# Optimization experiments

Measured on AMD Instinct MI355X. Metric: run time of the kernel, lower is better.

## Reference

```python
import jax, jax.numpy as jnp
import numpy as np

H = 4  # hidden_size
L = 2  # num_layers


def _lstm_cell(x, h, c, Wih, Whh, bih, bhh):
    # PyTorch gate order: input, forget, cell(g), output
    gates = x @ Wih.T + h @ Whh.T + (bih + bhh)  # [B, 4H]
    i, f, g, o = jnp.split(gates, 4, axis=-1)
    i = jax.nn.sigmoid(i)
    f = jax.nn.sigmoid(f)
    g = jnp.tanh(g)
    o = jax.nn.sigmoid(o)
    c_new = f * c + i * g
    h_new = o * jnp.tanh(c_new)
    return h_new, c_new


def setup_inputs() -> dict:
    key = jax.random.key(0)
    ks = jax.random.split(key, 24)
    B, S, D, T = 32768, 256, 8, 12
    s = 1.0 / np.sqrt(H)  # PyTorch LSTM init scale

    def u(k, shape):
        return jax.random.uniform(k, shape, jnp.float32, -s, s)

    inp = {
        "src": jax.random.normal(ks[0], (B, S, D), jnp.float32),
        "trg": jax.random.normal(ks[1], (B, T, 1), jnp.float32),
        # encoder LSTM (input_dim=8 -> H, then H -> H)
        "enc_Wih0": u(ks[2], (4 * H, D)), "enc_Whh0": u(ks[3], (4 * H, H)),
        "enc_bih0": u(ks[4], (4 * H,)), "enc_bhh0": u(ks[5], (4 * H,)),
        "enc_Wih1": u(ks[6], (4 * H, H)), "enc_Whh1": u(ks[7], (4 * H, H)),
        "enc_bih1": u(ks[8], (4 * H,)), "enc_bhh1": u(ks[9], (4 * H,)),
        # decoder LSTM (input_dim=1 -> H, then H -> H)
        "dec_Wih0": u(ks[10], (4 * H, 1)), "dec_Whh0": u(ks[11], (4 * H, H)),
        "dec_bih0": u(ks[12], (4 * H,)), "dec_bhh0": u(ks[13], (4 * H,)),
        "dec_Wih1": u(ks[14], (4 * H, H)), "dec_Whh1": u(ks[15], (4 * H, H)),
        "dec_bih1": u(ks[16], (4 * H,)), "dec_bhh1": u(ks[17], (4 * H,)),
        # fc: hidden -> 1
        "fc_W": u(ks[18], (1, H)), "fc_b": u(ks[19], (1,)),
    }
    return inp


def reference(src, trg,
              enc_Wih0, enc_Whh0, enc_bih0, enc_bhh0,
              enc_Wih1, enc_Whh1, enc_bih1, enc_bhh1,
              dec_Wih0, dec_Whh0, dec_bih0, dec_bhh0,
              dec_Wih1, dec_Whh1, dec_bih1, dec_bhh1,
              fc_W, fc_b):
    B, T = src.shape[0], trg.shape[1]
    enc_layers = [(enc_Wih0, enc_Whh0, enc_bih0, enc_bhh0),
                  (enc_Wih1, enc_Whh1, enc_bih1, enc_bhh1)]
    dec_layers = [(dec_Wih0, dec_Whh0, dec_bih0, dec_bhh0),
                  (dec_Wih1, dec_Whh1, dec_bih1, dec_bhh1)]

    def multi_step(layers, h, c, x):
        new_h, new_c, inp = [], [], x
        for l, p in enumerate(layers):
            hl, cl = _lstm_cell(inp, h[l], c[l], *p)
            new_h.append(hl); new_c.append(cl); inp = hl
        return jnp.stack(new_h), jnp.stack(new_c), inp

    # ---- encoder: scan over src time steps ----
    h0 = jnp.zeros((L, B, H), src.dtype)
    c0 = jnp.zeros((L, B, H), src.dtype)

    def enc_step(carry, x_t):
        h, c = carry
        h, c, _ = multi_step(enc_layers, h, c, x_t)
        return (h, c), None

    (h, c), _ = jax.lax.scan(enc_step, (h0, c0), jnp.swapaxes(src, 0, 1))

    x0 = trg[:, 0, :]  # [B, 1]

    def dec_step(carry, _):
        h, c, x = carry
        h, c, top = multi_step(dec_layers, h, c, x)
        pred = top @ fc_W.T + fc_b  # [B, 1]
        return (h, c, pred), pred

    _, preds = jax.lax.scan(dec_step, (h, c, x0), None, length=T - 1)  # [T-1, B, 1]
    outputs = jnp.concatenate([x0[None], preds], axis=0)  # [T, B, 1]
    return jnp.swapaxes(outputs, 0, 1)  # [B, T, 1]
```

## Files before the change

kernel.cpp:

```cpp
#include <hip/hip_runtime.h>

namespace {

constexpr int Sn = 256;
constexpr int Tn = 12;

__device__ __forceinline__ float rcp_(float x) { return __builtin_amdgcn_rcpf(x); }
__device__ __forceinline__ float sigm_(float x) { return rcp_(1.0f + __expf(-x)); }
__device__ __forceinline__ float tanh_(float x) { return 1.0f - 2.0f * rcp_(__expf(2.0f * x) + 1.0f); }

template <int CTRL>
__device__ __forceinline__ float qperm(float v) {
  return __int_as_float(
      __builtin_amdgcn_mov_dpp(__float_as_int(v), CTRL, 0xF, 0xF, true));
}
constexpr int DPP_XOR1 = 0xB1;
constexpr int DPP_XOR2 = 0x4E;
constexpr int DPP_XOR3 = 0x1B;
constexpr int DPP_BC0 = 0x00;

__device__ __forceinline__ float unit_update(const float* g, float& c) {
  float iv = sigm_(g[0]);
  float fv = sigm_(g[1]);
  float gv = tanh_(g[2]);
  float ov = sigm_(g[3]);
  c = fmaf(fv, c, iv * gv);
  return ov * tanh_(c);
}

__device__ __forceinline__ void quad_gather(float h, float* hg) {
  hg[0] = h;
  hg[1] = qperm<DPP_XOR1>(h);
  hg[2] = qperm<DPP_XOR2>(h);
  hg[3] = qperm<DPP_XOR3>(h);
}

__global__ __launch_bounds__(64) void seq2seq_kernel(
    const float* __restrict__ src, const float* __restrict__ trg,
    const float* __restrict__ eWih0, const float* __restrict__ eWhh0,
    const float* __restrict__ ebih0, const float* __restrict__ ebhh0,
    const float* __restrict__ eWih1, const float* __restrict__ eWhh1,
    const float* __restrict__ ebih1, const float* __restrict__ ebhh1,
    const float* __restrict__ dWih0, const float* __restrict__ dWhh0,
    const float* __restrict__ dbih0, const float* __restrict__ dbhh0,
    const float* __restrict__ dWih1, const float* __restrict__ dWhh1,
    const float* __restrict__ dbih1, const float* __restrict__ dbhh1,
    const float* __restrict__ fcW, const float* __restrict__ fcb,
    float* __restrict__ out) {
  const int gid = blockIdx.x * 64 + threadIdx.x;
  const int e = gid >> 2;
  const int u = gid & 3;

  float w0x[4][8], w0h[4][4], b0r[4];
  float w1i[4][4], w1h[4][4], b1r[4];
#pragma unroll
  for (int gi = 0; gi < 4; ++gi) {
    const int r = gi * 4 + u;
#pragma unroll
    for (int j = 0; j < 8; ++j) w0x[gi][j] = eWih0[r * 8 + j];
#pragma unroll
    for (int k = 0; k < 4; ++k) {
      w0h[gi][k] = eWhh0[r * 4 + (u ^ k)];
      w1i[gi][k] = eWih1[r * 4 + (u ^ k)];
      w1h[gi][k] = eWhh1[r * 4 + (u ^ k)];
    }
    b0r[gi] = ebih0[r] + ebhh0[r];
    b1r[gi] = ebih1[r] + ebhh1[r];
  }

  const float4* sp = (const float4*)(src + (size_t)e * (Sn * 8));

  float h0g[4] = {0, 0, 0, 0};
  float h1g[4] = {0, 0, 0, 0};
  float c0 = 0.0f, c1 = 0.0f;

  for (int t = 0; t < Sn; ++t) {
    float4 xa = sp[2 * t];
    float4 xb = sp[2 * t + 1];
    float x[8] = {xa.x, xa.y, xa.z, xa.w, xb.x, xb.y, xb.z, xb.w};
    float g[4];
#pragma unroll
    for (int gi = 0; gi < 4; ++gi) {
      float acc = b0r[gi];
#pragma unroll
      for (int j = 0; j < 8; ++j) acc = fmaf(x[j], w0x[gi][j], acc);
#pragma unroll
      for (int k = 0; k < 4; ++k) acc = fmaf(h0g[k], w0h[gi][k], acc);
      g[gi] = acc;
    }
    float h0 = unit_update(g, c0);
    quad_gather(h0, h0g);
#pragma unroll
    for (int gi = 0; gi < 4; ++gi) {
      float acc = b1r[gi];
#pragma unroll
      for (int k = 0; k < 4; ++k) acc = fmaf(h0g[k], w1i[gi][k], acc);
#pragma unroll
      for (int k = 0; k < 4; ++k) acc = fmaf(h1g[k], w1h[gi][k], acc);
      g[gi] = acc;
    }
    float h1 = unit_update(g, c1);
    quad_gather(h1, h1g);
  }

  float dw0i[4], dw0h[4][4], db0[4];
  float dw1i[4][4], dw1h[4][4], db1[4];
  float fcw[4];
#pragma unroll
  for (int gi = 0; gi < 4; ++gi) {
    const int r = gi * 4 + u;
    dw0i[gi] = dWih0[r];
#pragma unroll
    for (int k = 0; k < 4; ++k) {
      dw0h[gi][k] = dWhh0[r * 4 + (u ^ k)];
      dw1i[gi][k] = dWih1[r * 4 + (u ^ k)];
      dw1h[gi][k] = dWhh1[r * 4 + (u ^ k)];
    }
    db0[gi] = dbih0[r] + dbhh0[r];
    db1[gi] = dbih1[r] + dbhh1[r];
  }
#pragma unroll
  for (int k = 0; k < 4; ++k) fcw[k] = fcW[u ^ k];
  const float fcbv = fcb[0];

  float xv = trg[(size_t)e * Tn];
  if (u == 0) out[(size_t)e * Tn] = xv;

  for (int t = 1; t < Tn; ++t) {
    float g[4];
#pragma unroll
    for (int gi = 0; gi < 4; ++gi) {
      float acc = fmaf(xv, dw0i[gi], db0[gi]);
#pragma unroll
      for (int k = 0; k < 4; ++k) acc = fmaf(h0g[k], dw0h[gi][k], acc);
      g[gi] = acc;
    }
    float h0 = unit_update(g, c0);
    quad_gather(h0, h0g);
#pragma unroll
    for (int gi = 0; gi < 4; ++gi) {
      float acc = db1[gi];
#pragma unroll
      for (int k = 0; k < 4; ++k) acc = fmaf(h0g[k], dw1i[gi][k], acc);
#pragma unroll
      for (int k = 0; k < 4; ++k) acc = fmaf(h1g[k], dw1h[gi][k], acc);
      g[gi] = acc;
    }
    float h1 = unit_update(g, c1);
    quad_gather(h1, h1g);
    float pred = fcbv;
#pragma unroll
    for (int k = 0; k < 4; ++k) pred = fmaf(h1g[k], fcw[k], pred);
    pred = qperm<DPP_BC0>(pred);
    if (u == 0) out[(size_t)e * Tn + t] = pred;
    xv = pred;
  }
}

}

extern "C" void kernel_launch(void* const* d_in, const int* in_sizes, int n_in,
                              void* d_out, int out_size, void* d_ws, size_t ws_size,
                              hipStream_t stream) {
  const float* src = (const float*)d_in[0];
  const float* trg = (const float*)d_in[1];
  const float* eWih0 = (const float*)d_in[2];
  const float* eWhh0 = (const float*)d_in[3];
  const float* ebih0 = (const float*)d_in[4];
  const float* ebhh0 = (const float*)d_in[5];
  const float* eWih1 = (const float*)d_in[6];
  const float* eWhh1 = (const float*)d_in[7];
  const float* ebih1 = (const float*)d_in[8];
  const float* ebhh1 = (const float*)d_in[9];
  const float* dWih0 = (const float*)d_in[10];
  const float* dWhh0 = (const float*)d_in[11];
  const float* dbih0 = (const float*)d_in[12];
  const float* dbhh0 = (const float*)d_in[13];
  const float* dWih1 = (const float*)d_in[14];
  const float* dWhh1 = (const float*)d_in[15];
  const float* dbih1 = (const float*)d_in[16];
  const float* dbhh1 = (const float*)d_in[17];
  const float* fcW = (const float*)d_in[18];
  const float* fcb = (const float*)d_in[19];
  float* out = (float*)d_out;

  const int B = 32768;
  const int lanes = B * 4;
  const int block = 64;
  const int grid = lanes / block;
  seq2seq_kernel<<<grid, block, 0, stream>>>(
      src, trg, eWih0, eWhh0, ebih0, ebhh0, eWih1, eWhh1, ebih1, ebhh1,
      dWih0, dWhh0, dbih0, dbhh0, dWih1, dWhh1, dbih1, dbhh1, fcW, fcb, out);
}
```

Baseline: 544.1 us.

## Use packed FP32 FMA for LSTM gate math and prefetch next src step

Gate weights are regrouped into pairs (input/forget and cell/output) so the gate dot products run as packed two-wide FMAs (v_pk_fma_f32) instead of scalar FMAs, roughly halving the FMA instruction count per step. The encoder loop also loads the next time step's src vectors one iteration early to hide global-load latency behind compute. The costs are broadcast moves to build the packed operands, and more live registers from the prefetch and the paired weight layout.

```diff
diff --git a/kernel.cpp b/kernel.cpp
--- a/kernel.cpp
+++ b/kernel.cpp
@@ -4,6 +4,12 @@
 
 constexpr int Sn = 256;
 constexpr int Tn = 12;
+
+typedef float v2f __attribute__((ext_vector_type(2)));
+
+__device__ __forceinline__ v2f pkfma(v2f a, v2f b, v2f c) {
+  return __builtin_elementwise_fma(a, b, c);
+}
 
 __device__ __forceinline__ float rcp_(float x) { return __builtin_amdgcn_rcpf(x); }
 __device__ __forceinline__ float sigm_(float x) { return rcp_(1.0f + __expf(-x)); }
@@ -19,11 +25,11 @@
 constexpr int DPP_XOR3 = 0x1B;
 constexpr int DPP_BC0 = 0x00;
 
-__device__ __forceinline__ float unit_update(const float* g, float& c) {
-  float iv = sigm_(g[0]);
-  float fv = sigm_(g[1]);
-  float gv = tanh_(g[2]);
-  float ov = sigm_(g[3]);
+__device__ __forceinline__ float unit_update(v2f g01, v2f g23, float& c) {
+  float iv = sigm_(g01.x);
+  float fv = sigm_(g01.y);
+  float gv = tanh_(g23.x);
+  float ov = sigm_(g23.y);
   c = fmaf(fv, c, iv * gv);
   return ov * tanh_(c);
 }
@@ -51,22 +57,29 @@
   const int e = gid >> 2;
   const int u = gid & 3;
 
-  float w0x[4][8], w0h[4][4], b0r[4];
-  float w1i[4][4], w1h[4][4], b1r[4];
-#pragma unroll
-  for (int gi = 0; gi < 4; ++gi) {
-    const int r = gi * 4 + u;
-#pragma unroll
-    for (int j = 0; j < 8; ++j) w0x[gi][j] = eWih0[r * 8 + j];
-#pragma unroll
-    for (int k = 0; k < 4; ++k) {
-      w0h[gi][k] = eWhh0[r * 4 + (u ^ k)];
-      w1i[gi][k] = eWih1[r * 4 + (u ^ k)];
-      w1h[gi][k] = eWhh1[r * 4 + (u ^ k)];
-    }
-    b0r[gi] = ebih0[r] + ebhh0[r];
-    b1r[gi] = ebih1[r] + ebhh1[r];
-  }
+  const int ri = u, rf = 4 + u, rg = 8 + u, ro = 12 + u;
+
+  v2f w0x01[8], w0x23[8], w0h01[4], w0h23[4];
+  v2f w1i01[4], w1i23[4], w1h01[4], w1h23[4];
+#pragma unroll
+  for (int j = 0; j < 8; ++j) {
+    w0x01[j] = v2f{eWih0[ri * 8 + j], eWih0[rf * 8 + j]};
+    w0x23[j] = v2f{eWih0[rg * 8 + j], eWih0[ro * 8 + j]};
+  }
+#pragma unroll
+  for (int k = 0; k < 4; ++k) {
+    const int kc = u ^ k;
+    w0h01[k] = v2f{eWhh0[ri * 4 + kc], eWhh0[rf * 4 + kc]};
+    w0h23[k] = v2f{eWhh0[rg * 4 + kc], eWhh0[ro * 4 + kc]};
+    w1i01[k] = v2f{eWih1[ri * 4 + kc], eWih1[rf * 4 + kc]};
+    w1i23[k] = v2f{eWih1[rg * 4 + kc], eWih1[ro * 4 + kc]};
+    w1h01[k] = v2f{eWhh1[ri * 4 + kc], eWhh1[rf * 4 + kc]};
+    w1h23[k] = v2f{eWhh1[rg * 4 + kc], eWhh1[ro * 4 + kc]};
+  }
+  const v2f b0_01 = v2f{ebih0[ri] + ebhh0[ri], ebih0[rf] + ebhh0[rf]};
+  const v2f b0_23 = v2f{ebih0[rg] + ebhh0[rg], ebih0[ro] + ebhh0[ro]};
+  const v2f b1_01 = v2f{ebih1[ri] + ebhh1[ri], ebih1[rf] + ebhh1[rf]};
+  const v2f b1_23 = v2f{ebih1[rg] + ebhh1[rg], ebih1[ro] + ebhh1[ro]};
 
   const float4* sp = (const float4*)(src + (size_t)e * (Sn * 8));
 
@@ -74,51 +87,65 @@
   float h1g[4] = {0, 0, 0, 0};
   float c0 = 0.0f, c1 = 0.0f;
 
+  float4 xa = sp[0], xb = sp[1];
   for (int t = 0; t < Sn; ++t) {
-    float4 xa = sp[2 * t];
-    float4 xb = sp[2 * t + 1];
+    const int tn = (t < Sn - 1) ? t + 1 : t;
+    float4 na = sp[2 * tn];
+    float4 nb = sp[2 * tn + 1];
+
     float x[8] = {xa.x, xa.y, xa.z, xa.w, xb.x, xb.y, xb.z, xb.w};
-    float g[4];
-#pragma unroll
-    for (int gi = 0; gi < 4; ++gi) {
-      float acc = b0r[gi];
-#pragma unroll
-      for (int j = 0; j < 8; ++j) acc = fmaf(x[j], w0x[gi][j], acc);
-#pragma unroll
-      for (int k = 0; k < 4; ++k) acc = fmaf(h0g[k], w0h[gi][k], acc);
-      g[gi] = acc;
-    }
-    float h0 = unit_update(g, c0);
+    v2f a01 = b0_01, a23 = b0_23;
+#pragma unroll
+    for (int j = 0; j < 8; ++j) {
+      v2f xx = v2f{x[j], x[j]};
+      a01 = pkfma(xx, w0x01[j], a01);
+      a23 = pkfma(xx, w0x23[j], a23);
+    }
+#pragma unroll
+    for (int k = 0; k < 4; ++k) {
+      v2f hh = v2f{h0g[k], h0g[k]};
+      a01 = pkfma(hh, w0h01[k], a01);
+      a23 = pkfma(hh, w0h23[k], a23);
+    }
+    float h0 = unit_update(a01, a23, c0);
     quad_gather(h0, h0g);
-#pragma unroll
-    for (int gi = 0; gi < 4; ++gi) {
-      float acc = b1r[gi];
-#pragma unroll
-      for (int k = 0; k < 4; ++k) acc = fmaf(h0g[k], w1i[gi][k], acc);
-#pragma unroll
-      for (int k = 0; k < 4; ++k) acc = fmaf(h1g[k], w1h[gi][k], acc);
-      g[gi] = acc;
-    }
-    float h1 = unit_update(g, c1);
+
+    a01 = b1_01;
+    a23 = b1_23;
+#pragma unroll
+    for (int k = 0; k < 4; ++k) {
+      v2f hh0 = v2f{h0g[k], h0g[k]};
+      v2f hh1 = v2f{h1g[k], h1g[k]};
+      a01 = pkfma(hh0, w1i01[k], a01);
+      a23 = pkfma(hh0, w1i23[k], a23);
+      a01 = pkfma(hh1, w1h01[k], a01);
+      a23 = pkfma(hh1, w1h23[k], a23);
+    }
+    float h1 = unit_update(a01, a23, c1);
     quad_gather(h1, h1g);
-  }
-
-  float dw0i[4], dw0h[4][4], db0[4];
-  float dw1i[4][4], dw1h[4][4], db1[4];
+
+    xa = na;
+    xb = nb;
+  }
+
+  v2f dw0i01 = v2f{dWih0[ri], dWih0[rf]};
+  v2f dw0i23 = v2f{dWih0[rg], dWih0[ro]};
+  v2f dw0h01[4], dw0h23[4], dw1i01[4], dw1i23[4], dw1h01[4], dw1h23[4];
+#pragma unroll
+  for (int k = 0; k < 4; ++k) {
+    const int kc = u ^ k;
+    dw0h01[k] = v2f{dWhh0[ri * 4 + kc], dWhh0[rf * 4 + kc]};
+    dw0h23[k] = v2f{dWhh0[rg * 4 + kc], dWhh0[ro * 4 + kc]};
+    dw1i01[k] = v2f{dWih1[ri * 4 + kc], dWih1[rf * 4 + kc]};
+    dw1i23[k] = v2f{dWih1[rg * 4 + kc], dWih1[ro * 4 + kc]};
+    dw1h01[k] = v2f{dWhh1[ri * 4 + kc], dWhh1[rf * 4 + kc]};
+    dw1h23[k] = v2f{dWhh1[rg * 4 + kc], dWhh1[ro * 4 + kc]};
+  }
+  const v2f db0_01 = v2f{dbih0[ri] + dbhh0[ri], dbih0[rf] + dbhh0[rf]};
+  const v2f db0_23 = v2f{dbih0[rg] + dbhh0[rg], dbih0[ro] + dbhh0[ro]};
+  const v2f db1_01 = v2f{dbih1[ri] + dbhh1[ri], dbih1[rf] + dbhh1[rf]};
+  const v2f db1_23 = v2f{dbih1[rg] + dbhh1[rg], dbih1[ro] + dbhh1[ro]};
   float fcw[4];
-#pragma unroll
-  for (int gi = 0; gi < 4; ++gi) {
-    const int r = gi * 4 + u;
-    dw0i[gi] = dWih0[r];
-#pragma unroll
-    for (int k = 0; k < 4; ++k) {
-      dw0h[gi][k] = dWhh0[r * 4 + (u ^ k)];
-      dw1i[gi][k] = dWih1[r * 4 + (u ^ k)];
-      dw1h[gi][k] = dWhh1[r * 4 + (u ^ k)];
-    }
-    db0[gi] = dbih0[r] + dbhh0[r];
-    db1[gi] = dbih1[r] + dbhh1[r];
-  }
 #pragma unroll
   for (int k = 0; k < 4; ++k) fcw[k] = fcW[u ^ k];
   const float fcbv = fcb[0];
@@ -127,27 +154,32 @@
   if (u == 0) out[(size_t)e * Tn] = xv;
 
   for (int t = 1; t < Tn; ++t) {
-    float g[4];
-#pragma unroll
-    for (int gi = 0; gi < 4; ++gi) {
-      float acc = fmaf(xv, dw0i[gi], db0[gi]);
-#pragma unroll
-      for (int k = 0; k < 4; ++k) acc = fmaf(h0g[k], dw0h[gi][k], acc);
-      g[gi] = acc;
-    }
-    float h0 = unit_update(g, c0);
+    v2f xx = v2f{xv, xv};
+    v2f a01 = pkfma(xx, dw0i01, db0_01);
+    v2f a23 = pkfma(xx, dw0i23, db0_23);
+#pragma unroll
+    for (int k = 0; k < 4; ++k) {
+      v2f hh = v2f{h0g[k], h0g[k]};
+      a01 = pkfma(hh, dw0h01[k], a01);
+      a23 = pkfma(hh, dw0h23[k], a23);
+    }
+    float h0 = unit_update(a01, a23, c0);
     quad_gather(h0, h0g);
-#pragma unroll
-    for (int gi = 0; gi < 4; ++gi) {
-      float acc = db1[gi];
-#pragma unroll
-      for (int k = 0; k < 4; ++k) acc = fmaf(h0g[k], dw1i[gi][k], acc);
-#pragma unroll
-      for (int k = 0; k < 4; ++k) acc = fmaf(h1g[k], dw1h[gi][k], acc);
-      g[gi] = acc;
-    }
-    float h1 = unit_update(g, c1);
+
+    a01 = db1_01;
+    a23 = db1_23;
+#pragma unroll
+    for (int k = 0; k < 4; ++k) {
+      v2f hh0 = v2f{h0g[k], h0g[k]};
+      v2f hh1 = v2f{h1g[k], h1g[k]};
+      a01 = pkfma(hh0, dw1i01[k], a01);
+      a23 = pkfma(hh0, dw1i23[k], a23);
+      a01 = pkfma(hh1, dw1h01[k], a01);
+      a23 = pkfma(hh1, dw1h23[k], a23);
+    }
+    float h1 = unit_update(a01, a23, c1);
     quad_gather(h1, h1g);
+
     float pred = fcbv;
 #pragma unroll
     for (int k = 0; k < 4; ++k) pred = fmaf(h1g[k], fcw[k], pred);
```

New measurement: 475.9 us. 1.14x faster.
